# Kernel optimization log

Hardware: AMD Instinct MI355X
Metric: run time of the kernel (lower is better)

## Reference

```python
import math
import jax, jax.numpy as jnp
import numpy as np

WINDOW_SHAPE = [30, 30, 8]
DEPTH = 8
NUM_DIMS = 3
N_POINTS = 2_000_000
BATCH = 4
SPARSE_SHAPE = np.array([32, 512, 512], dtype=np.int64)  # [D, H, W]


def _right_shift_bits(b, k):
    # shift bit-array right along last axis: prepend k zeros, drop last k
    if b.shape[-1] <= k:
        return jnp.zeros_like(b)
    pad = [(0, 0)] * (b.ndim - 1) + [(k, 0)]
    return jnp.pad(b[..., :-k], pad)


def _gray2binary(gray):
    # prefix-XOR along last axis via doubling (matches torch gray2binary)
    n = gray.shape[-1]
    shift = 2 ** (math.ceil(math.log2(n)) - 1)
    while shift > 0:
        gray = jnp.logical_xor(gray, _right_shift_bits(gray, shift))
        shift //= 2
    return gray


def hilbert_encode(locs, num_dims, num_bits):
    # locs: [N, num_dims] int, each in [0, 2**num_bits)
    n = locs.shape[0]
    # bit b of gray is the (num_bits-1-b)-th bit of the coordinate (MSB first)
    shifts_ = (num_bits - 1 - jnp.arange(num_bits, dtype=locs.dtype))
    gray = ((locs[:, :, None] >> shifts_[None, None, :]) & 1).astype(bool)  # [N, D, B]
    # Skilling's transform: small fixed loop (num_bits*num_dims = 24 iters)
    for bit in range(num_bits):
        for dim in range(num_dims):
            mask = gray[:, dim, bit]  # [N]
            g0 = jnp.logical_xor(gray[:, 0, bit + 1:], mask[:, None])
            gray = gray.at[:, 0, bit + 1:].set(g0)
            to_flip = jnp.logical_and(
                jnp.logical_not(mask)[:, None],
                jnp.logical_xor(gray[:, 0, bit + 1:], gray[:, dim, bit + 1:]),
            )
            gray = gray.at[:, dim, bit + 1:].set(
                jnp.logical_xor(gray[:, dim, bit + 1:], to_flip))
            gray = gray.at[:, 0, bit + 1:].set(
                jnp.logical_xor(gray[:, 0, bit + 1:], to_flip))
    # interleave: swapaxes(1,2) then flatten -> [N, num_bits*num_dims], MSB first
    bits = jnp.transpose(gray, (0, 2, 1)).reshape(n, num_bits * num_dims)
    hb = _gray2binary(bits)
    nb = num_bits * num_dims
    weights = jnp.asarray((1 << (nb - 1 - np.arange(nb))), dtype=jnp.int32)
    code = (hb.astype(jnp.int32) * weights).sum(-1)
    return code


def setup_inputs() -> dict:
    key = jax.random.key(0)
    kb, kz, ky, kx = jax.random.split(key, 4)
    D, H, W = [int(v) for v in SPARSE_SHAPE]
    b = jax.random.randint(kb, (N_POINTS,), 0, BATCH, dtype=jnp.int32)
    z = jax.random.randint(kz, (N_POINTS,), 0, D, dtype=jnp.int32)
    y = jax.random.randint(ky, (N_POINTS,), 0, H, dtype=jnp.int32)
    x = jax.random.randint(kx, (N_POINTS,), 0, W, dtype=jnp.int32)
    coords = jnp.stack([b, z, y, x], axis=-1)  # [N, 4]: bs, z, y, x
    return {"coords": coords, "sparse_shape": SPARSE_SHAPE, "shifts": 1}


def reference(coords, sparse_shape, shifts):
    # sparse_shape is static config: [D, H, W]; reversed -> W, H, D (as in torch)
    ss = [int(v) for v in np.asarray(sparse_shape)][::-1]
    W, H, D = ss
    wx, wy, wz = WINDOW_SHAPE
    if bool(shifts):
        sx, sy, sz = math.ceil(wx / 2), math.ceil(wy / 2), math.ceil(wz / 2)
    else:
        sx = sy = sz = 0
    b = coords[:, 0]
    x = (coords[:, 3] + sx) % W
    y = (coords[:, 2] + sy) % H
    z = (coords[:, 1] + sz) % D
    locs = jnp.stack([x, y, z], axis=-1)  # [N, 3]
    code = hilbert_encode(locs, NUM_DIMS, DEPTH)
    code = code | (b.astype(code.dtype) << (DEPTH * 3))
    coords2curve = jnp.argsort(code)
    return coords2curve
```

## Files before the change

kernel.cpp:

```cpp
#include <hip/hip_runtime.h>
#include <stdint.h>


#define THREADS 512
#define TILE 4096
#define NBINS 512
#define RADIX_BITS 9
#define ROUNDS (TILE / THREADS)
#define WAVES (THREADS / 64)
#define CHUNK (TILE / WAVES)

__device__ __forceinline__ uint32_t hilbert_code(uint32_t x, uint32_t y, uint32_t z) {
  uint32_t X0 = x & 255u, X1 = y & 255u, X2 = z & 255u;
#pragma unroll
  for (int p = 7; p >= 0; --p) {
    uint32_t low = (1u << p) - 1u;
    uint32_t f0 = (uint32_t)-(int)((X0 >> p) & 1u);
    X0 ^= (low & f0);
    uint32_t f1 = (uint32_t)-(int)((X1 >> p) & 1u);
    uint32_t t1 = ((X0 ^ X1) & low) & ~f1;
    X0 ^= (low & f1) ^ t1;
    X1 ^= t1;
    uint32_t f2 = (uint32_t)-(int)((X2 >> p) & 1u);
    uint32_t t2 = ((X0 ^ X2) & low) & ~f2;
    X0 ^= (low & f2) ^ t2;
    X2 ^= t2;
  }
  uint32_t G = 0;
#pragma unroll
  for (int k = 0; k < 8; ++k) {
    int p = 7 - k;
    G |= ((X0 >> p) & 1u) << (23 - 3 * k);
    G |= ((X1 >> p) & 1u) << (22 - 3 * k);
    G |= ((X2 >> p) & 1u) << (21 - 3 * k);
  }
  G ^= G >> 16; G ^= G >> 8; G ^= G >> 4; G ^= G >> 2; G ^= G >> 1;
  return G & 0xFFFFFFu;
}

__global__ __launch_bounds__(THREADS) void genkeys_hist(
    const int4* __restrict__ coords, const void* __restrict__ ss,
    const int* __restrict__ shifts, uint64_t* __restrict__ pairs,
    int* __restrict__ hist, int N) {
  __shared__ int lh[NBINS];
  int t = threadIdx.x, b = blockIdx.x;
  if (t < NBINS) lh[t] = 0;

  const int* p32 = (const int*)ss;
  int D, H, W;
  if (p32[1] == 0) { const long long* p64 = (const long long*)ss;
    D = (int)p64[0]; H = (int)p64[1]; W = (int)p64[2]; }
  else { D = p32[0]; H = p32[1]; W = p32[2]; }
  int sflag = shifts[0];
  int sx = sflag ? 15 : 0, sy = sflag ? 15 : 0, sz = sflag ? 4 : 0;
  bool wp2 = (W & (W - 1)) == 0, hp2 = (H & (H - 1)) == 0, dp2 = (D & (D - 1)) == 0;
  __syncthreads();

#pragma unroll
  for (int r = 0; r < ROUNDS; ++r) {
    int idx = b * TILE + r * THREADS + t;
    if (idx < N) {
      int4 c = coords[idx];
      uint32_t bb = (uint32_t)c.x;
      int zz = c.y + sz, yy = c.z + sy, xx = c.w + sx;
      uint32_t z = (uint32_t)(dp2 ? (zz & (D - 1)) : (zz % D));
      uint32_t y = (uint32_t)(hp2 ? (yy & (H - 1)) : (yy % H));
      uint32_t x = (uint32_t)(wp2 ? (xx & (W - 1)) : (xx % W));
      uint32_t code = hilbert_code(x, y, z) | (bb << 24);
      pairs[idx] = ((uint64_t)(uint32_t)idx << 32) | code;
      atomicAdd(&lh[code & (NBINS - 1)], 1);
    }
  }
  __syncthreads();
  if (t < NBINS) hist[(size_t)b * NBINS + t] = lh[t];
}

template <int SHIFT>
__global__ __launch_bounds__(THREADS) void hist_kernel(
    const uint64_t* __restrict__ pairs, int* __restrict__ hist, int N) {
  __shared__ int lh[NBINS];
  int t = threadIdx.x, b = blockIdx.x;
  if (t < NBINS) lh[t] = 0;
  __syncthreads();
  const uint32_t* keys = (const uint32_t*)pairs;
#pragma unroll
  for (int r = 0; r < ROUNDS; ++r) {
    int idx = b * TILE + r * THREADS + t;
    if (idx < N) atomicAdd(&lh[(keys[(size_t)idx * 2] >> SHIFT) & (NBINS - 1)], 1);
  }
  __syncthreads();
  if (t < NBINS) hist[(size_t)b * NBINS + t] = lh[t];
}

__global__ __launch_bounds__(256) void scan_blocks(
    int* __restrict__ hist, int* __restrict__ digitTotals, int nblocks) {
  __shared__ int s[512];
  int d = blockIdx.x, t = threadIdx.x;
  int carry = 0;
  for (int start = 0; start < nblocks; start += 512) {
    int i0 = start + t, i1 = start + t + 256;
    int v0 = (i0 < nblocks) ? hist[(size_t)i0 * NBINS + d] : 0;
    int v1 = (i1 < nblocks) ? hist[(size_t)i1 * NBINS + d] : 0;
    s[t] = v0; s[t + 256] = v1;
    __syncthreads();
    for (int off = 1; off < 512; off <<= 1) {
      int a0 = (t >= off) ? s[t - off] : 0;
      int a1 = s[t + 256 - off];
      int b0 = s[t], b1 = s[t + 256];
      __syncthreads();
      s[t] = b0 + a0; s[t + 256] = b1 + a1;
      __syncthreads();
    }
    if (i0 < nblocks) hist[(size_t)i0 * NBINS + d] = carry + s[t] - v0;
    if (i1 < nblocks) hist[(size_t)i1 * NBINS + d] = carry + s[t + 256] - v1;
    int total = s[511];
    __syncthreads();
    carry += total;
  }
  if (t == 0) digitTotals[d] = carry;
}

template <int SHIFT, bool FINAL>
__global__ __launch_bounds__(THREADS) void scatter_kernel(
    const uint64_t* __restrict__ pairsIn,
    uint64_t* __restrict__ pairsOut, int* __restrict__ valsOut,
    const int* __restrict__ hist, const int* __restrict__ digitTotals,
    int N, int nblocks) {
  __shared__ uint64_t sbuf[TILE];
  __shared__ unsigned short cnt[WAVES][NBINS];
  __shared__ int digitStart[NBINS];
  __shared__ int adjArr[NBINS];
  __shared__ int2 wtot[WAVES];
  int t = threadIdx.x, b = blockIdx.x;
  int wave = t >> 6, lane = t & 63;

  int histv = 0, dt = 0;
  if (t < NBINS) {
    histv = hist[(size_t)b * NBINS + t];
    dt = digitTotals[t];
  }
#pragma unroll
  for (int w = 0; w < WAVES; ++w) cnt[w][t] = 0;
  __syncthreads();

  uint64_t kvR[ROUNDS];
  int drR[ROUNDS];
  uint64_t lt = (1ull << lane) - 1ull;
  int chunk0 = b * TILE + wave * CHUNK;

#pragma unroll
  for (int r = 0; r < ROUNDS; ++r) {
    int idx = chunk0 + r * 64 + lane;
    bool valid = idx < N;
    uint64_t kv = valid ? pairsIn[idx] : 0ull;
    kvR[r] = kv;
    int digit = (int)(((uint32_t)kv >> SHIFT) & (NBINS - 1));
    uint64_t eq = __ballot(valid);
#pragma unroll
    for (int bit = 0; bit < RADIX_BITS; ++bit) {
      uint64_t m = __ballot((digit >> bit) & 1);
      eq &= ((digit >> bit) & 1) ? m : ~m;
    }
    int waveRank = __popcll(eq & lt);
    int cntW = __popcll(eq);
    int prior = cnt[wave][digit];
    drR[r] = valid ? (digit | ((prior + waveRank) << RADIX_BITS)) : -1;
    if (valid && waveRank == 0) cnt[wave][digit] = (unsigned short)(prior + cntW);
  }
  __syncthreads();

  int tot = 0;
  {
#pragma unroll
    for (int w = 0; w < WAVES; ++w) {
      int x = cnt[w][t];
      cnt[w][t] = (unsigned short)tot;
      tot += x;
    }
  }

  {
    int2 v = make_int2(tot, dt);
#pragma unroll
    for (int off = 1; off < 64; off <<= 1) {
      int nx = __shfl_up(v.x, off);
      int ny = __shfl_up(v.y, off);
      if (lane >= off) { v.x += nx; v.y += ny; }
    }
    if (lane == 63) wtot[wave] = v;
    __syncthreads();
    int2 pre = make_int2(0, 0);
    for (int w = 0; w < wave; ++w) { pre.x += wtot[w].x; pre.y += wtot[w].y; }
    int ds = v.x + pre.x - tot;
    digitStart[t] = ds;
    adjArr[t] = histv + (v.y + pre.y - dt) - ds;
  }
  __syncthreads();

#pragma unroll
  for (int r = 0; r < ROUNDS; ++r) {
    int dr = drR[r];
    if (dr >= 0) {
      int digit = dr & (NBINS - 1);
      int rnk = dr >> RADIX_BITS;
      sbuf[digitStart[digit] + (int)cnt[wave][digit] + rnk] = kvR[r];
    }
  }
  __syncthreads();

  int validCount = min(TILE, N - b * TILE);
#pragma unroll
  for (int j = 0; j < ROUNDS; ++j) {
    int i = j * THREADS + t;
    if (i < validCount) {
      uint64_t kv = sbuf[i];
      int digit = (int)(((uint32_t)kv >> SHIFT) & (NBINS - 1));
      int pos = adjArr[digit] + i;
      if (FINAL) valsOut[pos] = (int)(kv >> 32);
      else pairsOut[pos] = kv;
    }
  }
}

extern "C" void kernel_launch(void* const* d_in, const int* in_sizes, int n_in,
                              void* d_out, int out_size, void* d_ws, size_t ws_size,
                              hipStream_t stream) {
  const int4* coords = (const int4*)d_in[0];
  const void* ss = d_in[1];
  const int* shifts = (const int*)d_in[2];
  int N = in_sizes[0] / 4;
  int nblocks = (N + TILE - 1) / TILE;

  char* ws = (char*)d_ws;
  size_t off = 0;
  auto alloc = [&](size_t bytes) -> void* {
    void* p = ws + off;
    off += (bytes + 255) & ~(size_t)255;
    return p;
  };
  uint64_t* pairsA = (uint64_t*)alloc((size_t)N * 8);
  uint64_t* pairsB = (uint64_t*)alloc((size_t)N * 8);
  int*      hist   = (int*)alloc((size_t)NBINS * nblocks * 4);
  int*      digitTotals = (int*)alloc(NBINS * 4);

  genkeys_hist<<<nblocks, THREADS, 0, stream>>>(coords, ss, shifts, pairsA, hist, N);
  scan_blocks<<<NBINS, 256, 0, stream>>>(hist, digitTotals, nblocks);
  scatter_kernel<0, false><<<nblocks, THREADS, 0, stream>>>(
      pairsA, pairsB, nullptr, hist, digitTotals, N, nblocks);

  hist_kernel<9><<<nblocks, THREADS, 0, stream>>>(pairsB, hist, N);
  scan_blocks<<<NBINS, 256, 0, stream>>>(hist, digitTotals, nblocks);
  scatter_kernel<9, false><<<nblocks, THREADS, 0, stream>>>(
      pairsB, pairsA, nullptr, hist, digitTotals, N, nblocks);

  hist_kernel<18><<<nblocks, THREADS, 0, stream>>>(pairsA, hist, N);
  scan_blocks<<<NBINS, 256, 0, stream>>>(hist, digitTotals, nblocks);
  scatter_kernel<18, true><<<nblocks, THREADS, 0, stream>>>(
      pairsA, nullptr, (int*)d_out, hist, digitTotals, N, nblocks);
}
```

Before: 90.30 us.

## Remap tiles per XCD, shrink final pass to 8 bits, shuffle-based scans

Adds a blockIdx-to-tile remap that gives each of the 8 XCDs a contiguous range of tiles, for L2 locality. The last radix pass now uses 256 bins, since the key tops out at bit 25, so it does less ballot and histogram work. The final scatter stages packed 32-bit digit|index words in LDS instead of 64-bit pairs. scan_blocks is rewritten to use wave shuffles and 512 threads, and the scatter kernel reuses shared buffers to cut LDS usage and raise occupancy. The risk is the added index arithmetic, plus correctness depending on N fitting in 23 bits and on the key range.

```diff
diff --git a/kernel.cpp b/kernel.cpp
--- a/kernel.cpp
+++ b/kernel.cpp
@@ -4,11 +4,15 @@
 
 #define THREADS 512
 #define TILE 4096
-#define NBINS 512
-#define RADIX_BITS 9
 #define ROUNDS (TILE / THREADS)
 #define WAVES (THREADS / 64)
 #define CHUNK (TILE / WAVES)
+
+__device__ __forceinline__ int tile_of(int bid, int nwg) {
+  int q = nwg >> 3, r = nwg & 7;
+  int x = bid & 7, k = bid >> 3;
+  return x * q + (x < r ? x : r) + k;
+}
 
 __device__ __forceinline__ uint32_t hilbert_code(uint32_t x, uint32_t y, uint32_t z) {
   uint32_t X0 = x & 255u, X1 = y & 255u, X2 = z & 255u;
@@ -42,9 +46,9 @@
     const int4* __restrict__ coords, const void* __restrict__ ss,
     const int* __restrict__ shifts, uint64_t* __restrict__ pairs,
     int* __restrict__ hist, int N) {
-  __shared__ int lh[NBINS];
-  int t = threadIdx.x, b = blockIdx.x;
-  if (t < NBINS) lh[t] = 0;
+  __shared__ int lh[512];
+  int t = threadIdx.x, b = tile_of(blockIdx.x, gridDim.x);
+  lh[t] = 0;
 
   const int* p32 = (const int*)ss;
   int D, H, W;
@@ -68,84 +72,80 @@
       uint32_t x = (uint32_t)(wp2 ? (xx & (W - 1)) : (xx % W));
       uint32_t code = hilbert_code(x, y, z) | (bb << 24);
       pairs[idx] = ((uint64_t)(uint32_t)idx << 32) | code;
-      atomicAdd(&lh[code & (NBINS - 1)], 1);
-    }
-  }
-  __syncthreads();
-  if (t < NBINS) hist[(size_t)b * NBINS + t] = lh[t];
-}
-
-template <int SHIFT>
+      atomicAdd(&lh[code & 511u], 1);
+    }
+  }
+  __syncthreads();
+  hist[(size_t)b * 512 + t] = lh[t];
+}
+
+template <int SHIFT, int NB>
 __global__ __launch_bounds__(THREADS) void hist_kernel(
     const uint64_t* __restrict__ pairs, int* __restrict__ hist, int N) {
-  __shared__ int lh[NBINS];
-  int t = threadIdx.x, b = blockIdx.x;
-  if (t < NBINS) lh[t] = 0;
+  __shared__ int lh[NB];
+  int t = threadIdx.x, b = tile_of(blockIdx.x, gridDim.x);
+  if (t < NB) lh[t] = 0;
   __syncthreads();
   const uint32_t* keys = (const uint32_t*)pairs;
 #pragma unroll
   for (int r = 0; r < ROUNDS; ++r) {
     int idx = b * TILE + r * THREADS + t;
-    if (idx < N) atomicAdd(&lh[(keys[(size_t)idx * 2] >> SHIFT) & (NBINS - 1)], 1);
-  }
-  __syncthreads();
-  if (t < NBINS) hist[(size_t)b * NBINS + t] = lh[t];
-}
-
-__global__ __launch_bounds__(256) void scan_blocks(
-    int* __restrict__ hist, int* __restrict__ digitTotals, int nblocks) {
-  __shared__ int s[512];
-  int d = blockIdx.x, t = threadIdx.x;
+    if (idx < N) atomicAdd(&lh[(keys[(size_t)idx * 2] >> SHIFT) & (NB - 1)], 1);
+  }
+  __syncthreads();
+  if (t < NB) hist[(size_t)b * NB + t] = lh[t];
+}
+
+__global__ __launch_bounds__(512) void scan_blocks(
+    int* __restrict__ hist, int* __restrict__ digitTotals, int nblocks, int nbins) {
+  __shared__ int wsum[8];
+  int d = blockIdx.x, t = threadIdx.x, wave = t >> 6, lane = t & 63;
   int carry = 0;
   for (int start = 0; start < nblocks; start += 512) {
-    int i0 = start + t, i1 = start + t + 256;
-    int v0 = (i0 < nblocks) ? hist[(size_t)i0 * NBINS + d] : 0;
-    int v1 = (i1 < nblocks) ? hist[(size_t)i1 * NBINS + d] : 0;
-    s[t] = v0; s[t + 256] = v1;
+    int i = start + t;
+    int vv = (i < nblocks) ? hist[(size_t)i * nbins + d] : 0;
+    int x = vv;
+#pragma unroll
+    for (int off = 1; off < 64; off <<= 1) {
+      int n = __shfl_up(x, off);
+      if (lane >= off) x += n;
+    }
+    if (lane == 63) wsum[wave] = x;
     __syncthreads();
-    for (int off = 1; off < 512; off <<= 1) {
-      int a0 = (t >= off) ? s[t - off] : 0;
-      int a1 = s[t + 256 - off];
-      int b0 = s[t], b1 = s[t + 256];
-      __syncthreads();
-      s[t] = b0 + a0; s[t + 256] = b1 + a1;
-      __syncthreads();
-    }
-    if (i0 < nblocks) hist[(size_t)i0 * NBINS + d] = carry + s[t] - v0;
-    if (i1 < nblocks) hist[(size_t)i1 * NBINS + d] = carry + s[t + 256] - v1;
-    int total = s[511];
+    int pre = 0;
+    for (int w = 0; w < wave; ++w) pre += wsum[w];
+    if (i < nblocks) hist[(size_t)i * nbins + d] = carry + pre + x - vv;
+    int tot = 0;
+    for (int w = 0; w < 8; ++w) tot += wsum[w];
     __syncthreads();
-    carry += total;
+    carry += tot;
   }
   if (t == 0) digitTotals[d] = carry;
 }
 
-template <int SHIFT, bool FINAL>
+template <int SHIFT, int NB, bool FINAL>
 __global__ __launch_bounds__(THREADS) void scatter_kernel(
     const uint64_t* __restrict__ pairsIn,
     uint64_t* __restrict__ pairsOut, int* __restrict__ valsOut,
     const int* __restrict__ hist, const int* __restrict__ digitTotals,
-    int N, int nblocks) {
-  __shared__ uint64_t sbuf[TILE];
-  __shared__ unsigned short cnt[WAVES][NBINS];
-  __shared__ int digitStart[NBINS];
-  __shared__ int adjArr[NBINS];
-  __shared__ int2 wtot[WAVES];
-  int t = threadIdx.x, b = blockIdx.x;
+    int N) {
+  constexpr int RB = (NB == 512) ? 9 : 8;
+  __shared__ uint64_t sbuf[FINAL ? TILE / 2 : TILE];
+  __shared__ __align__(16) unsigned short cnt[WAVES][NB];
+  int t = threadIdx.x, b = tile_of(blockIdx.x, gridDim.x);
   int wave = t >> 6, lane = t & 63;
 
   int histv = 0, dt = 0;
-  if (t < NBINS) {
-    histv = hist[(size_t)b * NBINS + t];
+  if (t < NB) {
+    histv = hist[(size_t)b * NB + t];
     dt = digitTotals[t];
   }
-#pragma unroll
-  for (int w = 0; w < WAVES; ++w) cnt[w][t] = 0;
+  for (int i = t; i < WAVES * NB; i += THREADS) ((unsigned short*)cnt)[i] = 0;
   __syncthreads();
 
   uint64_t kvR[ROUNDS];
   int drR[ROUNDS];
-  uint64_t lt = (1ull << lane) - 1ull;
+  uint64_t ltm = (1ull << lane) - 1ull;
   int chunk0 = b * TILE + wave * CHUNK;
 
 #pragma unroll
@@ -154,46 +154,48 @@
     bool valid = idx < N;
     uint64_t kv = valid ? pairsIn[idx] : 0ull;
     kvR[r] = kv;
-    int digit = (int)(((uint32_t)kv >> SHIFT) & (NBINS - 1));
+    int digit = (int)(((uint32_t)kv >> SHIFT) & (NB - 1));
     uint64_t eq = __ballot(valid);
 #pragma unroll
-    for (int bit = 0; bit < RADIX_BITS; ++bit) {
+    for (int bit = 0; bit < RB; ++bit) {
       uint64_t m = __ballot((digit >> bit) & 1);
       eq &= ((digit >> bit) & 1) ? m : ~m;
     }
-    int waveRank = __popcll(eq & lt);
+    int waveRank = __popcll(eq & ltm);
     int cntW = __popcll(eq);
     int prior = cnt[wave][digit];
-    drR[r] = valid ? (digit | ((prior + waveRank) << RADIX_BITS)) : -1;
+    drR[r] = valid ? (digit | ((prior + waveRank) << RB)) : -1;
     if (valid && waveRank == 0) cnt[wave][digit] = (unsigned short)(prior + cntW);
   }
   __syncthreads();
 
-  int tot = 0;
-  {
+  int2* wt = (int2*)sbuf;
+  int tot = 0, adjv = 0;
+  int2 v = make_int2(0, 0);
+  if (t < NB) {
+#pragma unroll
+    for (int w = 0; w < WAVES; ++w) tot += cnt[w][t];
+    v = make_int2(tot, dt);
+#pragma unroll
+    for (int off = 1; off < 64; off <<= 1) {
+      int nx = __shfl_up(v.x, off), ny = __shfl_up(v.y, off);
+      if (lane >= off) { v.x += nx; v.y += ny; }
+    }
+    if (lane == 63) wt[wave] = v;
+  }
+  __syncthreads();
+  if (t < NB) {
+    int2 pre = make_int2(0, 0);
+    for (int w = 0; w < wave; ++w) { pre.x += wt[w].x; pre.y += wt[w].y; }
+    int ds = pre.x + v.x - tot;
+    adjv = histv + (pre.y + v.y - dt) - ds;
+    int run = ds;
 #pragma unroll
     for (int w = 0; w < WAVES; ++w) {
       int x = cnt[w][t];
-      cnt[w][t] = (unsigned short)tot;
-      tot += x;
-    }
-  }
-
-  {
-    int2 v = make_int2(tot, dt);
-#pragma unroll
-    for (int off = 1; off < 64; off <<= 1) {
-      int nx = __shfl_up(v.x, off);
-      int ny = __shfl_up(v.y, off);
-      if (lane >= off) { v.x += nx; v.y += ny; }
-    }
-    if (lane == 63) wtot[wave] = v;
-    __syncthreads();
-    int2 pre = make_int2(0, 0);
-    for (int w = 0; w < wave; ++w) { pre.x += wtot[w].x; pre.y += wtot[w].y; }
-    int ds = v.x + pre.x - tot;
-    digitStart[t] = ds;
-    adjArr[t] = histv + (v.y + pre.y - dt) - ds;
+      cnt[w][t] = (unsigned short)run;
+      run += x;
+    }
   }
   __syncthreads();
 
@@ -201,11 +203,19 @@
   for (int r = 0; r < ROUNDS; ++r) {
     int dr = drR[r];
     if (dr >= 0) {
-      int digit = dr & (NBINS - 1);
-      int rnk = dr >> RADIX_BITS;
-      sbuf[digitStart[digit] + (int)cnt[wave][digit] + rnk] = kvR[r];
-    }
-  }
+      int digit = dr & (NB - 1);
+      int rnk = dr >> RB;
+      int slot = (int)cnt[wave][digit] + rnk;
+      if (FINAL)
+        ((uint32_t*)sbuf)[slot] = ((uint32_t)digit << 23) | (uint32_t)(kvR[r] >> 32);
+      else
+        sbuf[slot] = kvR[r];
+    }
+  }
+  __syncthreads();
+
+  int* adjArr = (int*)cnt;
+  if (t < NB) adjArr[t] = adjv;
   __syncthreads();
 
   int validCount = min(TILE, N - b * TILE);
@@ -213,11 +223,15 @@
   for (int j = 0; j < ROUNDS; ++j) {
     int i = j * THREADS + t;
     if (i < validCount) {
-      uint64_t kv = sbuf[i];
-      int digit = (int)(((uint32_t)kv >> SHIFT) & (NBINS - 1));
-      int pos = adjArr[digit] + i;
-      if (FINAL) valsOut[pos] = (int)(kv >> 32);
-      else pairsOut[pos] = kv;
+      if (FINAL) {
+        uint32_t pk = ((uint32_t*)sbuf)[i];
+        int digit = (int)(pk >> 23);
+        valsOut[adjArr[digit] + i] = (int)(pk & 0x7FFFFFu);
+      } else {
+        uint64_t kv = sbuf[i];
+        int digit = (int)(((uint32_t)kv >> SHIFT) & (NB - 1));
+        pairsOut[adjArr[digit] + i] = kv;
+      }
     }
   }
 }
@@ -240,21 +254,21 @@
   };
   uint64_t* pairsA = (uint64_t*)alloc((size_t)N * 8);
   uint64_t* pairsB = (uint64_t*)alloc((size_t)N * 8);
-  int*      hist   = (int*)alloc((size_t)NBINS * nblocks * 4);
-  int*      digitTotals = (int*)alloc(NBINS * 4);
+  int*      hist   = (int*)alloc((size_t)512 * nblocks * 4);
+  int*      digitTotals = (int*)alloc(512 * 4);
 
   genkeys_hist<<<nblocks, THREADS, 0, stream>>>(coords, ss, shifts, pairsA, hist, N);
-  scan_blocks<<<NBINS, 256, 0, stream>>>(hist, digitTotals, nblocks);
-  scatter_kernel<0, false><<<nblocks, THREADS, 0, stream>>>(
-      pairsA, pairsB, nullptr, hist, digitTotals, N, nblocks);
-
-  hist_kernel<9><<<nblocks, THREADS, 0, stream>>>(pairsB, hist, N);
-  scan_blocks<<<NBINS, 256, 0, stream>>>(hist, digitTotals, nblocks);
-  scatter_kernel<9, false><<<nblocks, THREADS, 0, stream>>>(
-      pairsB, pairsA, nullptr, hist, digitTotals, N, nblocks);
-
-  hist_kernel<18><<<nblocks, THREADS, 0, stream>>>(pairsA, hist, N);
-  scan_blocks<<<NBINS, 256, 0, stream>>>(hist, digitTotals, nblocks);
-  scatter_kernel<18, true><<<nblocks, THREADS, 0, stream>>>(
-      pairsA, nullptr, (int*)d_out, hist, digitTotals, N, nblocks);
-}
+  scan_blocks<<<512, 512, 0, stream>>>(hist, digitTotals, nblocks, 512);
+  scatter_kernel<0, 512, false><<<nblocks, THREADS, 0, stream>>>(
+      pairsA, pairsB, nullptr, hist, digitTotals, N);
+
+  hist_kernel<9, 512><<<nblocks, THREADS, 0, stream>>>(pairsB, hist, N);
+  scan_blocks<<<512, 512, 0, stream>>>(hist, digitTotals, nblocks, 512);
+  scatter_kernel<9, 512, false><<<nblocks, THREADS, 0, stream>>>(
+      pairsB, pairsA, nullptr, hist, digitTotals, N);
+
+  hist_kernel<18, 256><<<nblocks, THREADS, 0, stream>>>(pairsA, hist, N);
+  scan_blocks<<<256, 512, 0, stream>>>(hist, digitTotals, nblocks, 256);
+  scatter_kernel<18, 256, true><<<nblocks, THREADS, 0, stream>>>(
+      pairsA, nullptr, (int*)d_out, hist, digitTotals, N);
+}
```

Result: faster. 85.02 us (-5.9%).
